# Kernel tuning notes

Hardware: AMD Instinct MI355X
Metric: run time of the kernel (lower is better)

## Reference

```python
import jax, jax.numpy as jnp
import numpy as np
from jax import lax

NUM_CLASSES = 80
TOPK = 1000
CONF_THRESH = 0.05
NMS_THRESH = 0.6
MAX_COORD = 4096.0  # > any box coordinate; used for class-aware NMS offset trick
N_ANCHORS = 262144


def setup_inputs() -> dict:
    key = jax.random.key(0)
    k1, k2, k3 = jax.random.split(key, 3)
    # classification logits; shift down so sigmoid scores are mostly below conf_thresh
    cls_pred = jax.random.normal(k1, (1, N_ANCHORS, NUM_CLASSES), jnp.float32) * 2.0 - 2.0
    # valid xyxy boxes in absolute pixel coords (image ~1024)
    xy = jax.random.uniform(k2, (1, N_ANCHORS, 2), jnp.float32) * 1000.0
    wh = jax.random.uniform(k3, (1, N_ANCHORS, 2), jnp.float32) * 200.0 + 4.0
    box_pred = jnp.concatenate([xy, xy + wh], axis=-1)
    return {"cls_pred": cls_pred, "box_pred": box_pred, "img_h": 1024, "img_w": 1024}


def _pairwise_iou(b):
    # b: [K, 4] xyxy -> [K, K] IoU
    x1, y1, x2, y2 = b[:, 0], b[:, 1], b[:, 2], b[:, 3]
    area = (x2 - x1) * (y2 - y1)
    ix1 = jnp.maximum(x1[:, None], x1[None, :])
    iy1 = jnp.maximum(y1[:, None], y1[None, :])
    ix2 = jnp.minimum(x2[:, None], x2[None, :])
    iy2 = jnp.minimum(y2[:, None], y2[None, :])
    inter = jnp.clip(ix2 - ix1, 0.0) * jnp.clip(iy2 - iy1, 0.0)
    return inter / (area[:, None] + area[None, :] - inter + 1e-9)


def reference(cls_pred, box_pred, img_h, img_w):
    cls_p = cls_pred[0]          # [N, C]
    box_p = box_pred[0]          # [N, 4]
    # sigmoid + flatten + descending sort + slice(topk)  ==  top_k on flat scores
    scores_all = jax.nn.sigmoid(cls_p).reshape(-1)            # [N*C]
    top_scores, top_idxs = lax.top_k(scores_all, TOPK)        # sorted descending
    valid = top_scores > CONF_THRESH                          # keep mask (fixed size)
    labels = top_idxs % NUM_CLASSES
    anchor_idxs = top_idxs // NUM_CLASSES
    boxes = box_p[anchor_idxs]                                # [K, 4]

    # class-aware (per-class) greedy NMS via coordinate offset trick
    offset = labels.astype(boxes.dtype)[:, None] * MAX_COORD
    iou = _pairwise_iou(boxes + offset)                       # [K, K]
    idx = jnp.arange(TOPK)

    def body(i, keep):
        sup = keep[i] & (iou[i] > NMS_THRESH) & (idx > i)
        return keep & ~sup

    keep = lax.fori_loop(0, TOPK, body, valid)

    # normalize boxes to [0, 1] by image size and clip (as inference_single_image)
    scale = jnp.array([img_w, img_h, img_w, img_h], dtype=boxes.dtype)
    boxes_norm = jnp.clip(boxes / scale, 0.0, 1.0)

    scores_out = jnp.where(keep, top_scores, 0.0)
    return boxes_norm, scores_out, labels, keep
```

## Files before the change

### kernel.cpp

```cpp
#include <hip/hip_runtime.h>
#include <stdint.h>

#define NUM_CLASSES 80u
#define TOPK 1000
#define CONF_T 0.05f
#define NMS_T 0.6f
#define MAX_COORD 4096.0f
#define TARGET 1152u
#define NBLK_A 2048u
#define SLOTS 48u
#define LINCAP (NBLK_A * SLOTS)
#define SRVCAP 2048u
#define STATIC_F 4.0f
#define STATIC_KEY 0xC0800000u
#define NBINS 4096
#define BINSH 13
#define LCAP 64u
#define PBLK 1536u

typedef unsigned long long ull;
typedef ull ull2 __attribute__((ext_vector_type(2)));

__device__ __forceinline__ uint32_t fkey(float x) {
  uint32_t k = __float_as_uint(x);
  return (k & 0x80000000u) ? ~k : (k | 0x80000000u);
}

__device__ __forceinline__ uint32_t suffix_scan_1024(uint32_t v, uint32_t* part,
                                                     int t) {
  int lane = t & 63, wid = t >> 6;
#pragma unroll
  for (int off = 1; off < 64; off <<= 1) {
    uint32_t x = __shfl_down(v, off);
    if (lane + off < 64) v += x;
  }
  if (lane == 0) part[wid] = v;
  __syncthreads();
  if (wid == 0) {
    uint32_t pv = (lane < 16) ? part[lane] : 0u;
#pragma unroll
    for (int off = 1; off < 16; off <<= 1) {
      uint32_t x = __shfl_down(pv, off);
      if (lane + off < 16) pv += x;
    }
    if (lane < 16) part[lane] = pv;
  }
  __syncthreads();
  uint32_t after = (wid < 15) ? part[wid + 1] : 0u;
  return v + after;
}

template <int NBINSX>
__device__ __forceinline__ void pick_bin1024(const uint32_t* hl, uint32_t target,
                                             int t, uint32_t* part,
                                             uint32_t* binS, uint32_t* AS,
                                             uint32_t* cntS) {
  const int CH = NBINSX / 1024;
  uint32_t cc[CH];
  uint32_t s = 0;
#pragma unroll
  for (int j = 0; j < CH; ++j) { cc[j] = hl[t * CH + j]; s += cc[j]; }
  uint32_t incl = suffix_scan_1024(s, part, t);
  uint32_t after = incl - s;
  if (incl >= target && after < target) {
    uint32_t cum = after;
    for (int j = CH - 1; j >= 0; --j) {
      if (cum + cc[j] >= target) {
        *binS = (uint32_t)(t * CH + j); *AS = cum; *cntS = cc[j]; break;
      }
      cum += cc[j];
    }
  }
}

__global__ void __launch_bounds__(256) kA(const float4* __restrict__ cls, int n4,
                                          uint32_t* __restrict__ sel,
                                          uint32_t* __restrict__ cnt,
                                          uint32_t* __restrict__ candKey,
                                          uint32_t* __restrict__ candIdx) {
  __shared__ uint32_t lk[LCAP];
  __shared__ uint32_t li[LCAP];
  __shared__ uint32_t lcnt;
  if (threadIdx.x == 0) lcnt = 0u;
  if (blockIdx.x == 0 && threadIdx.x < 16) sel[threadIdx.x] = 0u;
  __syncthreads();
  int stride = gridDim.x * blockDim.x;
  for (int i = blockIdx.x * blockDim.x + threadIdx.x; i < n4; i += stride) {
    float4 v = cls[i];
    float f4[4] = {v.x, v.y, v.z, v.w};
#pragma unroll
    for (int c = 0; c < 4; ++c) {
      if (f4[c] >= STATIC_F) {
        uint32_t p = atomicAdd(&lcnt, 1u);
        if (p < LCAP) { lk[p] = fkey(f4[c]); li[p] = (uint32_t)i * 4u + c; }
      }
    }
  }
  __syncthreads();
  uint32_t c = lcnt;
  if (threadIdx.x == 0) cnt[blockIdx.x] = c;
  uint32_t m = c; if (m > SLOTS) m = SLOTS;
  uint32_t base = blockIdx.x * SLOTS;
  for (uint32_t i = threadIdx.x; i < SLOTS; i += 256u)
    candKey[base + i] = (i < m) ? lk[i] : 0u;
  for (uint32_t i = threadIdx.x; i < m; i += 256u)
    candIdx[base + i] = li[i];
}

__global__ void __launch_bounds__(1024) kSel(
    const float4* __restrict__ cls4, int n4,
    uint32_t* __restrict__ sel, const uint32_t* __restrict__ cnt,
    const uint32_t* __restrict__ candKey, const uint32_t* __restrict__ candIdx,
    ull* __restrict__ srv, float* __restrict__ out,
    float* __restrict__ topScore) {
  __shared__ uint32_t hl[NBINS];
  __shared__ uint32_t part[16];
  __shared__ uint32_t sk_[PBLK];
  __shared__ uint32_t si_[PBLK];
  __shared__ uint32_t lcnt, gbase, binS, AS, cntS, ovS;
  int t = threadIdx.x;
  uint32_t b = blockIdx.x;

  uint32_t c0 = cnt[t], c1 = cnt[t + 1024];
  if (t == 0) { lcnt = 0u; binS = 0u; AS = 0u; cntS = 0u; ovS = 0u; }
  for (int i = t; i < NBINS; i += 1024) hl[i] = 0u;
  __syncthreads();
  if (c0 > SLOTS || c1 > SLOTS) atomicOr(&ovS, 1u);
  uint32_t m0 = c0 > SLOTS ? SLOTS : c0, m1 = c1 > SLOTS ? SLOTS : c1;
  (void)suffix_scan_1024(m0 + m1, part, t);
  uint32_t total = part[0];
  bool fb = (ovS != 0u) || (total < TARGET);

  if (!fb) {
    const uint4* ck4 = (const uint4*)candKey;
    for (uint32_t i = t; i < LINCAP / 4u; i += 1024u) {
      uint4 kv = ck4[i];
      uint32_t kk[4] = {kv.x, kv.y, kv.z, kv.w};
#pragma unroll
      for (int q = 0; q < 4; ++q) {
        uint32_t k = kk[q];
        if (k >= STATIC_KEY) {
          uint32_t bb = (k - STATIC_KEY) >> BINSH;
          if (bb > NBINS - 1u) bb = NBINS - 1u;
          atomicAdd(&hl[bb], 1u);
        }
      }
    }
    __syncthreads();
    pick_bin1024<NBINS>(hl, TARGET, t, part, &binS, &AS, &cntS);
    __syncthreads();
    bool bump = (AS + cntS > SRVCAP);
    uint32_t T = STATIC_KEY + ((binS + (bump ? 1u : 0u)) << BINSH);
    if (bump && b == 0) {
      for (int i = t; i < 4000; i += 1024) out[i] = 0.0f;
      for (int i = t; i < 1000; i += 1024) { out[5000 + i] = 0.0f; topScore[i] = 0.0f; }
    }
    uint32_t lo = b * (LINCAP / 64u), hi = lo + (LINCAP / 64u);
    for (uint32_t i = lo + t; i < hi; i += 1024u) {
      uint32_t k = candKey[i];
      if (k >= T) {
        uint32_t p = atomicAdd(&lcnt, 1u);
        sk_[p] = k; si_[p] = candIdx[i];
      }
    }
    __syncthreads();
    uint32_t c = lcnt;
    if (t == 0 && c) gbase = atomicAdd(&sel[4], c);
    __syncthreads();
    for (uint32_t i = t; i < c; i += 1024u) {
      uint32_t k = sk_[i];
      float x = __uint_as_float(k & 0x7fffffffu);
      float p = 1.0f / (1.0f + expf(-x));
      uint32_t pos = gbase + i;
      if (pos < SRVCAP)
        srv[pos] = ((ull)__float_as_uint(p) << 32) | (ull)(uint32_t)(~si_[i]);
    }
  } else {
    if (b != 0) return;
    for (int i = t; i < NBINS; i += 1024) hl[i] = 0u;
    if (t == 0) { binS = 0u; AS = 0u; cntS = 0u; }
    __syncthreads();
    for (int i = t; i < n4; i += 1024) {
      float4 v = cls4[i];
      atomicAdd(&hl[fkey(v.x) >> 20], 1u);
      atomicAdd(&hl[fkey(v.y) >> 20], 1u);
      atomicAdd(&hl[fkey(v.z) >> 20], 1u);
      atomicAdd(&hl[fkey(v.w) >> 20], 1u);
    }
    __syncthreads();
    pick_bin1024<NBINS>(hl, TARGET, t, part, &binS, &AS, &cntS);
    __syncthreads();
    uint32_t b20 = binS, A = AS;
    hl[t] = 0u;
    if (t == 0) binS = 0u;
    __syncthreads();
    for (int i = t; i < n4; i += 1024) {
      float4 v = cls4[i];
      uint32_t k4[4] = {fkey(v.x), fkey(v.y), fkey(v.z), fkey(v.w)};
#pragma unroll
      for (int c2 = 0; c2 < 4; ++c2)
        if ((k4[c2] >> 20) == b20) atomicAdd(&hl[(k4[c2] >> 10) & 1023u], 1u);
    }
    __syncthreads();
    uint32_t rem = TARGET - A;
    pick_bin1024<1024>(hl, rem, t, part, &binS, &AS, &cntS);
    __syncthreads();
    uint32_t T = (b20 << 20) | (binS << 10);
    for (int i = t; i < 4000; i += 1024) out[i] = 0.0f;
    for (int i = t; i < 1000; i += 1024) { out[5000 + i] = 0.0f; topScore[i] = 0.0f; }
    for (int i = t; i < n4; i += 1024) {
      float4 v = cls4[i];
      uint32_t k4[4] = {fkey(v.x), fkey(v.y), fkey(v.z), fkey(v.w)};
#pragma unroll
      for (int c2 = 0; c2 < 4; ++c2) {
        uint32_t k = k4[c2];
        if (k >= T) {
          uint32_t pos = atomicAdd(&sel[4], 1u);
          if (pos < SRVCAP) {
            float x = (k & 0x80000000u) ? __uint_as_float(k & 0x7fffffffu)
                                        : __uint_as_float(~k);
            float p = 1.0f / (1.0f + expf(-x));
            uint32_t idx = (uint32_t)i * 4u + c2;
            srv[pos] = ((ull)__float_as_uint(p) << 32) | (ull)(uint32_t)(~idx);
          }
        }
      }
    }
  }
}

__global__ void __launch_bounds__(256) kF2(
    const float* __restrict__ box, const int* __restrict__ ph,
    const int* __restrict__ pw, const uint32_t* __restrict__ sel,
    const ull* __restrict__ srv, float* __restrict__ out,
    float* __restrict__ topScore, float* __restrict__ obox) {
  __shared__ __align__(16) ull sk[SRVCAP];
  int t = threadIdx.x;
  uint32_t scount = sel[4]; if (scount > SRVCAP) scount = SRVCAP;
  uint32_t pad = (scount + 1u) & ~1u;
  for (uint32_t i = t; i < pad; i += 256u) sk[i] = (i < scount) ? srv[i] : 0ull;
  __syncthreads();
  uint32_t i = blockIdx.x * 256u + (uint32_t)t;
  if (i >= scount) return;
  ull my = sk[i];
  uint32_t rank = 0;
#pragma unroll 4
  for (uint32_t j = 0; j < pad; j += 2u) {
    ull2 v = *reinterpret_cast<const ull2*>(&sk[j]);
    rank += (v.x > my) + (v.y > my);
  }
  if (rank >= TOPK) return;
  uint32_t idx = ~(uint32_t)my;
  float p = __uint_as_float((uint32_t)(my >> 32));
  uint32_t label = idx % NUM_CLASSES;
  uint32_t anchor = idx / NUM_CLASSES;
  float W = (float)pw[0], H = (float)ph[0];
  float b0 = box[anchor * 4u + 0u], b1 = box[anchor * 4u + 1u];
  float b2 = box[anchor * 4u + 2u], b3 = box[anchor * 4u + 3u];
  out[rank * 4 + 0] = fminf(fmaxf(b0 / W, 0.0f), 1.0f);
  out[rank * 4 + 1] = fminf(fmaxf(b1 / H, 0.0f), 1.0f);
  out[rank * 4 + 2] = fminf(fmaxf(b2 / W, 0.0f), 1.0f);
  out[rank * 4 + 3] = fminf(fmaxf(b3 / H, 0.0f), 1.0f);
  out[5000 + rank] = (float)label;
  topScore[rank] = p;
  float off = (float)label * MAX_COORD;
  obox[rank * 4 + 0] = b0 + off; obox[rank * 4 + 1] = b1 + off;
  obox[rank * 4 + 2] = b2 + off; obox[rank * 4 + 3] = b3 + off;
}

__global__ void kG(const float* __restrict__ obox, ull* __restrict__ masks,
                   uint32_t* __restrict__ rowsum) {
  __shared__ uint32_t rsS;
  int i = blockIdx.x;
  if (threadIdx.x == 0) rsS = 0u;
  __syncthreads();
  float x1i = obox[i * 4 + 0], y1i = obox[i * 4 + 1];
  float x2i = obox[i * 4 + 2], y2i = obox[i * 4 + 3];
  float ai = (x2i - x1i) * (y2i - y1i);
  for (int base = 0; base < 1024; base += 256) {
    int jj = base + (int)threadIdx.x;
    bool bit = false;
    if (jj < TOPK && jj > i) {
      float x1j = obox[jj * 4 + 0], y1j = obox[jj * 4 + 1];
      float x2j = obox[jj * 4 + 2], y2j = obox[jj * 4 + 3];
      float aj = (x2j - x1j) * (y2j - y1j);
      float ix1 = fmaxf(x1i, x1j), iy1 = fmaxf(y1i, y1j);
      float ix2 = fminf(x2i, x2j), iy2 = fminf(y2i, y2j);
      float iw = fmaxf(ix2 - ix1, 0.0f), ih = fmaxf(iy2 - iy1, 0.0f);
      float inter = iw * ih;
      float iou = inter / (ai + aj - inter + 1e-9f);
      bit = iou > NMS_T;
    }
    ull m = __ballot(bit);
    if ((threadIdx.x & 63u) == 0u) {
      masks[i * 16 + (jj >> 6)] = m;
      if (m) atomicOr(&rsS, 1u << (jj >> 6));
    }
  }
  __syncthreads();
  if (threadIdx.x == 0) rowsum[i] = rsS;
}

__global__ void __launch_bounds__(1024) kH(const float* __restrict__ topScore,
                                           const ull* __restrict__ masks,
                                           const uint32_t* __restrict__ rowsum,
                                           float* __restrict__ out) {
  __shared__ ull lmask[TOPK * 16];
  __shared__ uint32_t rsL[TOPK];
  __shared__ ull keepsh[16];
  int t = threadIdx.x;
  if (t < TOPK) rsL[t] = rowsum[t];
  if (t < 16) keepsh[t] = 0ull;
  __syncthreads();
  for (int i = t; i < TOPK * 16; i += 1024)
    lmask[i] = ((rsL[i >> 4] >> (i & 15)) & 1u) ? masks[i] : 0ull;
  {
    bool v = (t < TOPK) && (topScore[t] > CONF_T);
    ull bb = __ballot(v);
    if ((t & 63) == 0) keepsh[t >> 6] = bb;
  }
  __syncthreads();
  if (t < 64) {
    ull kw = (t < 16) ? keepsh[t] : 0ull;
    ull nzw = 0ull;
    if (t < 16) {
      for (int b = 0; b < 64; ++b) {
        int r = t * 64 + b;
        if (r < TOPK && rsL[r]) nzw |= 1ull << b;
      }
    }
    for (int w = 0; w < 16; ++w) {
      ull cur = __shfl(kw, w) & __shfl(nzw, w);
      while (cur) {
        int b = __ffsll((long long)cur) - 1;
        int i = w * 64 + b;
        if (t < 16) kw &= ~lmask[i * 16 + t];
        ull nk = __shfl(kw, w);
        cur = nk & __shfl(nzw, w);
        cur &= (b == 63) ? 0ull : (~0ull << (b + 1));
      }
    }
    if (t < 16) keepsh[t] = kw;
  }
  __syncthreads();
  if (t < TOPK) {
    bool k = (keepsh[t >> 6] >> (t & 63)) & 1ull;
    float s = topScore[t];
    out[4000 + t] = k ? s : 0.0f;
    out[6000 + t] = k ? 1.0f : 0.0f;
  }
}

extern "C" void kernel_launch(void* const* d_in, const int* in_sizes, int n_in,
                              void* d_out, int out_size, void* d_ws, size_t ws_size,
                              hipStream_t stream) {
  const float* cls = (const float*)d_in[0];
  const float* box = (const float*)d_in[1];
  const int* ph = (const int*)d_in[2];
  const int* pw = (const int*)d_in[3];
  float* out = (float*)d_out;
  int n = in_sizes[0];

  uint8_t* w = (uint8_t*)d_ws;
  uint32_t* cnt     = (uint32_t*)(w);
  uint32_t* sel     = (uint32_t*)(w + 8192);
  uint32_t* candKey = (uint32_t*)(w + 12288);
  uint32_t* candIdx = (uint32_t*)(w + 12288 + (size_t)LINCAP * 4);
  ull*      srv     = (ull*)     (w + 12288 + (size_t)LINCAP * 8);
  float*    topScore= (float*)   (w + 12288 + (size_t)LINCAP * 8 + 16384);
  float*    obox    = (float*)   (w + 12288 + (size_t)LINCAP * 8 + 16384 + 4096);
  ull*      masks   = (ull*)     (w + 12288 + (size_t)LINCAP * 8 + 16384 + 4096 + 16384);
  uint32_t* rowsum  = (uint32_t*)(w + 12288 + (size_t)LINCAP * 8 + 16384 + 4096 + 16384 + 131072);

  kA  <<<NBLK_A, 256, 0, stream>>>((const float4*)cls, n / 4, sel, cnt, candKey, candIdx);
  kSel<<<64, 1024, 0, stream>>>((const float4*)cls, n / 4, sel, cnt, candKey, candIdx, srv, out, topScore);
  kF2 <<<SRVCAP / 256, 256, 0, stream>>>(box, ph, pw, sel, srv, out, topScore, obox);
  kG  <<<TOPK, 256, 0, stream>>>(obox, masks, rowsum);
  kH  <<<1, 1024, 0, stream>>>(topScore, masks, rowsum, out);
}
```

Before: 169.1 us.

## Fuse top-k ranking, box gather and IoU mask kernels into one launch

Merges the rank/gather kernel and the pairwise IoU mask kernel into a single 16-block kernel. Each block redundantly ranks all survivors and gathers the top boxes into shared memory, then computes 63 rows of the suppression bitmask with one thread per 64-bit word. This removes a kernel launch and the global round-trip of the offset boxes. In exchange, every block repeats the O(n^2) rank computation, and the mask computation is now serial per word rather than wave-parallel with ballot.

```diff
diff --git a/kernel.cpp b/kernel.cpp
--- a/kernel.cpp
+++ b/kernel.cpp
@@ -17,6 +17,7 @@
 #define BINSH 13
 #define LCAP 64u
 #define PBLK 1536u
+#define ROWS_PB 63u
 
 typedef unsigned long long ull;
 typedef ull ull2 __attribute__((ext_vector_type(2)));
@@ -229,76 +230,91 @@
   }
 }
 
-__global__ void __launch_bounds__(256) kF2(
+__global__ void __launch_bounds__(1024) kFG(
     const float* __restrict__ box, const int* __restrict__ ph,
     const int* __restrict__ pw, const uint32_t* __restrict__ sel,
     const ull* __restrict__ srv, float* __restrict__ out,
-    float* __restrict__ topScore, float* __restrict__ obox) {
+    float* __restrict__ topScore, ull* __restrict__ masks,
+    uint32_t* __restrict__ rowsum) {
   __shared__ __align__(16) ull sk[SRVCAP];
+  __shared__ float ob[TOPK][4];
+  __shared__ uint32_t rkslot[TOPK];
+  __shared__ uint32_t rs[ROWS_PB];
   int t = threadIdx.x;
+  uint32_t b = blockIdx.x;
   uint32_t scount = sel[4]; if (scount > SRVCAP) scount = SRVCAP;
   uint32_t pad = (scount + 1u) & ~1u;
-  for (uint32_t i = t; i < pad; i += 256u) sk[i] = (i < scount) ? srv[i] : 0ull;
-  __syncthreads();
-  uint32_t i = blockIdx.x * 256u + (uint32_t)t;
-  if (i >= scount) return;
-  ull my = sk[i];
-  uint32_t rank = 0;
-#pragma unroll 4
-  for (uint32_t j = 0; j < pad; j += 2u) {
-    ull2 v = *reinterpret_cast<const ull2*>(&sk[j]);
-    rank += (v.x > my) + (v.y > my);
-  }
-  if (rank >= TOPK) return;
-  uint32_t idx = ~(uint32_t)my;
-  float p = __uint_as_float((uint32_t)(my >> 32));
-  uint32_t label = idx % NUM_CLASSES;
-  uint32_t anchor = idx / NUM_CLASSES;
+  for (uint32_t i = t; i < pad; i += 1024u) sk[i] = (i < scount) ? srv[i] : 0ull;
+  if (t < (int)ROWS_PB) rs[t] = 0u;
+  __syncthreads();
+  for (uint32_t s = t; s < scount; s += 1024u) {
+    ull my = sk[s];
+    uint32_t rank = 0;
+    for (uint32_t j = 0; j < pad; j += 2u) {
+      ull2 v = *reinterpret_cast<const ull2*>(&sk[j]);
+      rank += (v.x > my) + (v.y > my);
+    }
+    if (rank < TOPK) rkslot[rank] = s;
+  }
+  __syncthreads();
   float W = (float)pw[0], H = (float)ph[0];
-  float b0 = box[anchor * 4u + 0u], b1 = box[anchor * 4u + 1u];
-  float b2 = box[anchor * 4u + 2u], b3 = box[anchor * 4u + 3u];
-  out[rank * 4 + 0] = fminf(fmaxf(b0 / W, 0.0f), 1.0f);
-  out[rank * 4 + 1] = fminf(fmaxf(b1 / H, 0.0f), 1.0f);
-  out[rank * 4 + 2] = fminf(fmaxf(b2 / W, 0.0f), 1.0f);
-  out[rank * 4 + 3] = fminf(fmaxf(b3 / H, 0.0f), 1.0f);
-  out[5000 + rank] = (float)label;
-  topScore[rank] = p;
-  float off = (float)label * MAX_COORD;
-  obox[rank * 4 + 0] = b0 + off; obox[rank * 4 + 1] = b1 + off;
-  obox[rank * 4 + 2] = b2 + off; obox[rank * 4 + 3] = b3 + off;
-}
-
-__global__ void kG(const float* __restrict__ obox, ull* __restrict__ masks,
-                   uint32_t* __restrict__ rowsum) {
-  __shared__ uint32_t rsS;
-  int i = blockIdx.x;
-  if (threadIdx.x == 0) rsS = 0u;
-  __syncthreads();
-  float x1i = obox[i * 4 + 0], y1i = obox[i * 4 + 1];
-  float x2i = obox[i * 4 + 2], y2i = obox[i * 4 + 3];
-  float ai = (x2i - x1i) * (y2i - y1i);
-  for (int base = 0; base < 1024; base += 256) {
-    int jj = base + (int)threadIdx.x;
-    bool bit = false;
-    if (jj < TOPK && jj > i) {
-      float x1j = obox[jj * 4 + 0], y1j = obox[jj * 4 + 1];
-      float x2j = obox[jj * 4 + 2], y2j = obox[jj * 4 + 3];
-      float aj = (x2j - x1j) * (y2j - y1j);
-      float ix1 = fmaxf(x1i, x1j), iy1 = fmaxf(y1i, y1j);
-      float ix2 = fminf(x2i, x2j), iy2 = fminf(y2i, y2j);
-      float iw = fmaxf(ix2 - ix1, 0.0f), ih = fmaxf(iy2 - iy1, 0.0f);
-      float inter = iw * ih;
-      float iou = inter / (ai + aj - inter + 1e-9f);
-      bit = iou > NMS_T;
-    }
-    ull m = __ballot(bit);
-    if ((threadIdx.x & 63u) == 0u) {
-      masks[i * 16 + (jj >> 6)] = m;
-      if (m) atomicOr(&rsS, 1u << (jj >> 6));
-    }
-  }
-  __syncthreads();
-  if (threadIdx.x == 0) rowsum[i] = rsS;
+  uint32_t nrank = scount < TOPK ? scount : TOPK;
+  for (uint32_t r = t; r < nrank; r += 1024u) {
+    uint32_t s = rkslot[r];
+    uint32_t idx = ~(uint32_t)sk[s];
+    uint32_t label = idx % NUM_CLASSES;
+    uint32_t anchor = idx / NUM_CLASSES;
+    float off = (float)label * MAX_COORD;
+    ob[r][0] = box[anchor * 4u + 0u] + off;
+    ob[r][1] = box[anchor * 4u + 1u] + off;
+    ob[r][2] = box[anchor * 4u + 2u] + off;
+    ob[r][3] = box[anchor * 4u + 3u] + off;
+    rkslot[r] = s | (label << 16);
+  }
+  __syncthreads();
+  uint32_t r0 = b * ROWS_PB;
+  uint32_t r1 = r0 + ROWS_PB; if (r1 > TOPK) r1 = TOPK;
+  for (uint32_t r = r0 + (uint32_t)t; r < r1; r += 1024u) {
+    if (r < nrank) {
+      uint32_t sl = rkslot[r];
+      uint32_t s = sl & 0xFFFFu;
+      uint32_t label = sl >> 16;
+      float off = (float)label * MAX_COORD;
+      float p = __uint_as_float((uint32_t)(sk[s] >> 32));
+      out[r * 4 + 0] = fminf(fmaxf((ob[r][0] - off) / W, 0.0f), 1.0f);
+      out[r * 4 + 1] = fminf(fmaxf((ob[r][1] - off) / H, 0.0f), 1.0f);
+      out[r * 4 + 2] = fminf(fmaxf((ob[r][2] - off) / W, 0.0f), 1.0f);
+      out[r * 4 + 3] = fminf(fmaxf((ob[r][3] - off) / H, 0.0f), 1.0f);
+      out[5000 + r] = (float)label;
+      topScore[r] = p;
+    }
+  }
+  uint32_t ntask = (r1 - r0) * 16u;
+  for (uint32_t task = t; task < ntask; task += 1024u) {
+    uint32_t rl = task >> 4, w = task & 15u;
+    uint32_t r = r0 + rl;
+    ull m = 0ull;
+    if (r < nrank) {
+      float x1i = ob[r][0], y1i = ob[r][1], x2i = ob[r][2], y2i = ob[r][3];
+      float ai = (x2i - x1i) * (y2i - y1i);
+      uint32_t jhi = w * 64u + 64u; if (jhi > nrank) jhi = nrank;
+      for (uint32_t j = w * 64u; j < jhi; ++j) {
+        if (j <= r) continue;
+        float x1j = ob[j][0], y1j = ob[j][1], x2j = ob[j][2], y2j = ob[j][3];
+        float aj = (x2j - x1j) * (y2j - y1j);
+        float ix1 = fmaxf(x1i, x1j), iy1 = fmaxf(y1i, y1j);
+        float ix2 = fminf(x2i, x2j), iy2 = fminf(y2i, y2j);
+        float iw = fmaxf(ix2 - ix1, 0.0f), ih = fmaxf(iy2 - iy1, 0.0f);
+        float inter = iw * ih;
+        float iou = inter / (ai + aj - inter + 1e-9f);
+        if (iou > NMS_T) m |= 1ull << (j & 63u);
+      }
+    }
+    masks[r * 16 + w] = m;
+    if (m) atomicOr(&rs[rl], 1u << w);
+  }
+  __syncthreads();
+  if (t < (int)(r1 - r0)) rowsum[r0 + t] = rs[t];
 }
 
 __global__ void __launch_bounds__(1024) kH(const float* __restrict__ topScore,
@@ -368,13 +384,11 @@
   uint32_t* candIdx = (uint32_t*)(w + 12288 + (size_t)LINCAP * 4);
   ull*      srv     = (ull*)     (w + 12288 + (size_t)LINCAP * 8);
   float*    topScore= (float*)   (w + 12288 + (size_t)LINCAP * 8 + 16384);
-  float*    obox    = (float*)   (w + 12288 + (size_t)LINCAP * 8 + 16384 + 4096);
-  ull*      masks   = (ull*)     (w + 12288 + (size_t)LINCAP * 8 + 16384 + 4096 + 16384);
-  uint32_t* rowsum  = (uint32_t*)(w + 12288 + (size_t)LINCAP * 8 + 16384 + 4096 + 16384 + 131072);
+  ull*      masks   = (ull*)     (w + 12288 + (size_t)LINCAP * 8 + 16384 + 4096);
+  uint32_t* rowsum  = (uint32_t*)(w + 12288 + (size_t)LINCAP * 8 + 16384 + 4096 + 131072);
 
   kA  <<<NBLK_A, 256, 0, stream>>>((const float4*)cls, n / 4, sel, cnt, candKey, candIdx);
   kSel<<<64, 1024, 0, stream>>>((const float4*)cls, n / 4, sel, cnt, candKey, candIdx, srv, out, topScore);
-  kF2 <<<SRVCAP / 256, 256, 0, stream>>>(box, ph, pw, sel, srv, out, topScore, obox);
-  kG  <<<TOPK, 256, 0, stream>>>(obox, masks, rowsum);
+  kFG <<<16, 1024, 0, stream>>>(box, ph, pw, sel, srv, out, topScore, masks, rowsum);
   kH  <<<1, 1024, 0, stream>>>(topScore, masks, rowsum, out);
 }
```

New measurement: 201.2 us. 1.19x slower.
